# Performance work log

Measured on AMD Instinct MI355X. Metric: run time of the kernel, lower is better.

The kernel has to match this reference:

```python
import jax, jax.numpy as jnp
import numpy as np


def setup_inputs() -> dict:
    key = jax.random.key(0)
    k1, k2 = jax.random.split(key)
    B, N, D, O = 16, 2048, 512, 512
    x = jax.random.normal(k1, (B, N, D), dtype=jnp.float32)
    # original uses nn.init.uniform_ -> U[0,1)
    kernel = jax.random.uniform(k2, (3, D, O), dtype=jnp.float32)
    return {"x": x, "kernel": kernel}


def reference(x, kernel):
    # x: [B, N, D], kernel: [3, D, O]
    O = kernel.shape[-1]
    q = jnp.einsum("bnd,do->bno", x, kernel[0])
    k = jnp.einsum("bnd,do->bno", x, kernel[1])
    v = jnp.einsum("bnd,do->bno", x, kernel[2])
    scores = jnp.einsum("bqo,bko->bqk", q, k) / jnp.sqrt(jnp.float32(O))
    attn = jax.nn.softmax(scores, axis=-1)  # [B, N, N]
    return jnp.einsum("bqk,bko->bqo", attn, v)
```

## Files before the change

### kernel.cpp

```cpp
#include <hip/hip_runtime.h>
#include <hip/hip_bf16.h>

typedef __bf16 bf16_t;
typedef _Float16 f16_t;
typedef __bf16 bf16x8 __attribute__((ext_vector_type(8)));
typedef _Float16 f16x8 __attribute__((ext_vector_type(8)));
typedef float  f32x4  __attribute__((ext_vector_type(4)));

#define GAS __attribute__((address_space(1)))
#define LAS __attribute__((address_space(3)))

__device__ __forceinline__ void gload_lds16(const void* g, void* l) {
    __builtin_amdgcn_global_load_lds((const GAS void*)g, (LAS void*)l, 16, 0, 0);
}

#define QSCALE 0.044194173824159216f
#define L2E    1.4426950408889634f

__global__ __launch_bounds__(256) void k_split_x(const float* __restrict__ X,
                                                 bf16_t* __restrict__ H,
                                                 bf16_t* __restrict__ L, int n) {
    int i = (blockIdx.x * 256 + threadIdx.x) * 4;
    if (i >= n) return;
    float4 v = *(const float4*)(X + i);
    float vv[4] = {v.x, v.y, v.z, v.w};
    union { bf16_t b[4]; uint2 u; } hh, ll;
#pragma unroll
    for (int j = 0; j < 4; j++) {
        bf16_t h = (bf16_t)vv[j];
        hh.b[j] = h;
        ll.b[j] = (bf16_t)(vv[j] - (float)h);
    }
    *(uint2*)(H + i) = hh.u;
    *(uint2*)(L + i) = ll.u;
}

__global__ __launch_bounds__(256) void k_split_wt(const float* __restrict__ W,
                                                  bf16_t* __restrict__ H,
                                                  bf16_t* __restrict__ L) {
    int t = blockIdx.x * 256 + threadIdx.x;
    int base = t * 4;
    int m = base >> 18;
    int o = (base >> 9) & 511;
    int d = base & 511;
    union { bf16_t b[4]; uint2 u; } hh, ll;
#pragma unroll
    for (int j = 0; j < 4; j++) {
        float w = W[m * 262144 + (d + j) * 512 + o];
        bf16_t h = (bf16_t)w;
        hh.b[j] = h;
        ll.b[j] = (bf16_t)(w - (float)h);
    }
    *(uint2*)(H + base) = hh.u;
    *(uint2*)(L + base) = ll.u;
}

__global__ __launch_bounds__(256) void k_qkv(
    const bf16_t* __restrict__ Ah, const bf16_t* __restrict__ Al,
    const bf16_t* __restrict__ Bh, const bf16_t* __restrict__ Bl,
    f16_t* __restrict__ Qf,
    f16_t* __restrict__ Kh, f16_t* __restrict__ Kl,
    bf16_t* __restrict__ VT) {
    __shared__ bf16_t lds[16384];
    bf16_t* As_h = lds;
    bf16_t* Bs_h = lds + 4096;
    bf16_t* As_l = lds + 8192;
    bf16_t* Bs_l = lds + 12288;

    const int tid = threadIdx.x;
    const int lane = tid & 63;
    const int wid = tid >> 6;
    const int wr = wid >> 1, wc = wid & 1;
    const size_t i0 = (size_t)blockIdx.y * 128;
    const size_t j0 = (size_t)blockIdx.x * 128;

    const bf16_t* pAh = Ah + i0 * 512;
    const bf16_t* pBh = Bh + j0 * 512;
    const bf16_t* pAl = Al + i0 * 512;
    const bf16_t* pBl = Bl + j0 * 512;

    const int srow = tid >> 2;
    const int scoff = (tid & 3) * 8;

    f32x4 acc[4][4] = {};

    const int arow = wr * 64 + (lane & 15);
    const int brow = wc * 64 + (lane & 15);
    const int ko = (lane >> 4) * 8;

    for (int kt = 0; kt < 512; kt += 32) {
#pragma unroll
        for (int c = 0; c < 2; c++) {
            const size_t ra = (size_t)(c * 64 + srow) * 512 + kt + scoff;
            const int loff = c * 2048 + tid * 8;
            gload_lds16(pAh + ra, As_h + loff);
            gload_lds16(pBh + ra, Bs_h + loff);
            gload_lds16(pAl + ra, As_l + loff);
            gload_lds16(pBl + ra, Bs_l + loff);
        }
        __syncthreads();

        bf16x8 ah[4], bh[4], al[4], bl[4];
#pragma unroll
        for (int m = 0; m < 4; m++) ah[m] = *(const bf16x8*)&As_h[(arow + m * 16) * 32 + ko];
#pragma unroll
        for (int n = 0; n < 4; n++) bh[n] = *(const bf16x8*)&Bs_h[(brow + n * 16) * 32 + ko];
#pragma unroll
        for (int m = 0; m < 4; m++) al[m] = *(const bf16x8*)&As_l[(arow + m * 16) * 32 + ko];
#pragma unroll
        for (int n = 0; n < 4; n++) bl[n] = *(const bf16x8*)&Bs_l[(brow + n * 16) * 32 + ko];
        __builtin_amdgcn_s_setprio(1);
#pragma unroll
        for (int m = 0; m < 4; m++)
#pragma unroll
            for (int n = 0; n < 4; n++) {
                acc[m][n] = __builtin_amdgcn_mfma_f32_16x16x32_bf16(ah[m], bh[n], acc[m][n], 0, 0, 0);
                acc[m][n] = __builtin_amdgcn_mfma_f32_16x16x32_bf16(ah[m], bl[n], acc[m][n], 0, 0, 0);
                acc[m][n] = __builtin_amdgcn_mfma_f32_16x16x32_bf16(al[m], bh[n], acc[m][n], 0, 0, 0);
            }
        __builtin_amdgcn_s_setprio(0);
        __syncthreads();
    }

#pragma unroll
    for (int m = 0; m < 4; m++) {
#pragma unroll
        for (int n = 0; n < 4; n++) {
#pragma unroll
            for (int j = 0; j < 4; j++) {
                const size_t gr = i0 + wr * 64 + m * 16 + (lane >> 4) * 4 + j;
                const size_t gc = j0 + wc * 64 + n * 16 + (lane & 15);
                float v = acc[m][n][j];
                const int mat = (int)(gc >> 9);
                const size_t bloc = gr >> 11;
                const size_t nrow = gr & 2047;
                const size_t o = gc & 511;
                const size_t idx = bloc * 1048576 + nrow * 512 + o;
                if (mat == 0) {
                    Qf[idx] = (f16_t)(v * QSCALE);
                } else if (mat == 1) {
                    f16_t h = (f16_t)v;
                    Kh[idx] = h; Kl[idx] = (f16_t)(v - (float)h);
                } else {
                    VT[bloc * 1048576 + o * 2048 + nrow] = (bf16_t)v;
                }
            }
        }
    }
}

#define KB_SZ   32768
#define VT_OFF  65536
#define PT_OFF  131072
#define MP_OFF  139264
#define SP_OFF  139776
#define MR_OFF  140288

__global__ __launch_bounds__(512) void k_flash(
    const f16_t* __restrict__ Qf,
    const f16_t* __restrict__ Kh, const f16_t* __restrict__ Kl,
    const bf16_t* __restrict__ VT, float* __restrict__ Out) {
    __shared__ __align__(16) char smem[140800];

    const int tid = threadIdx.x;
    const int l = tid & 63, wid = tid >> 6;
    const int l15 = l & 15, l4 = l >> 4;
    const int rg4 = wid >> 1, kg = wid & 1;
    const int rg2 = wid >> 2, cg = wid & 3;

    const int total = gridDim.x * gridDim.y;
    const int f = blockIdx.x + gridDim.x * blockIdx.y;
    const int fp = (f & 7) * (total >> 3) + (f >> 3);
    const int b = fp >> 5;
    const int q0 = (fp & 31) * 64;
    const size_t NB = 1048576;

    const f16_t* qfb = Qf + (size_t)b * NB;
    const f16_t* khb = Kh + (size_t)b * NB;
    const f16_t* klb = Kl + (size_t)b * NB;
    const bf16_t* vtb = VT + (size_t)b * NB;

    float* MP = (float*)(smem + MP_OFF);
    float* SP = (float*)(smem + SP_OFF);
    float* MR = (float*)(smem + MR_OFF);

    if (tid < 128) MR[tid] = -3e38f;

    f32x4 O[2][8] = {};
    float mreg[2][4], lreg[2][4];
#pragma unroll
    for (int mf = 0; mf < 2; mf++)
#pragma unroll
        for (int j = 0; j < 4; j++) { mreg[mf][j] = -3e38f; lreg[mf][j] = 0.f; }

    const int srow = tid >> 3;
    const int sgl = (tid & 7) ^ (srow & 7);
    const int gsw = l15 & 7;

    auto stage_k = [&](int t, int kc2, int b2) {
#pragma unroll
        for (int sub = 0; sub < 2; sub++) {
            const int co = kc2 * 128 + sub * 64 + sgl * 8;
            f16_t* d = (f16_t*)(smem + b2 * KB_SZ + sub * 16384) + tid * 8;
            gload_lds16(khb + (size_t)(t * 64 + srow) * 512 + co, d);
            gload_lds16(klb + (size_t)(t * 64 + srow) * 512 + co, d + 4096);
        }
    };
    auto stage_v = [&](int t, int j) {
        const int g = j * 512 + tid;
        const int orow = g >> 3;
        const int gl = (g & 7) ^ (orow & 7);
        gload_lds16(vtb + (size_t)orow * 2048 + t * 64 + gl * 8,
                    (bf16_t*)(smem + VT_OFF + g * 16));
    };

#pragma unroll
    for (int qc = 0; qc < 8; qc++) {
        const int co = qc * 64 + sgl * 8;
        gload_lds16(qfb + (size_t)(q0 + srow) * 512 + co,
                    (f16_t*)(smem + VT_OFF + qc * 8192) + tid * 8);
    }
    stage_k(0, 0, 0);
    asm volatile("s_waitcnt vmcnt(4)" ::: "memory");
    __builtin_amdgcn_s_barrier();

    f16x8 qreg[16];
    const int arow = rg4 * 16 + l15;
#pragma unroll
    for (int qc = 0; qc < 8; qc++)
#pragma unroll
        for (int ks = 0; ks < 2; ks++) {
            const int gph = ((ks * 4 + l4) ^ gsw) << 4;
            qreg[qc * 2 + ks] = *(const f16x8*)(smem + VT_OFF + qc * 8192 + arow * 128 + gph);
        }
    asm volatile("s_waitcnt lgkmcnt(0)" ::: "memory");
    __builtin_amdgcn_s_barrier();

#pragma unroll 1
    for (int t = 0; t < 32; t++) {
        f32x4 S[2] = {};
#pragma unroll
        for (int kc2 = 0; kc2 < 4; kc2++) {
            if (kc2 == 0) asm volatile("s_waitcnt vmcnt(0)" ::: "memory");
            else          asm volatile("s_waitcnt vmcnt(2)" ::: "memory");
            __builtin_amdgcn_s_barrier();
            if (kc2 < 3) {
                stage_k(t, kc2 + 1, (kc2 + 1) & 1);
                stage_v(t, kc2 * 2);
                stage_v(t, kc2 * 2 + 1);
            } else {
                stage_v(t, 6);
                stage_v(t, 7);
                if (t < 31) stage_k(t + 1, 0, 0);
            }
            const char* CB = smem + (kc2 & 1) * KB_SZ;
#pragma unroll
            for (int sub = 0; sub < 2; sub++)
#pragma unroll
                for (int ks = 0; ks < 2; ks++) {
                    const int gph = ((ks * 4 + l4) ^ gsw) << 4;
                    f16x8 qa = qreg[kc2 * 4 + sub * 2 + ks];
                    __builtin_amdgcn_s_setprio(1);
#pragma unroll
                    for (int nf = 0; nf < 2; nf++) {
                        const int brow = kg * 32 + nf * 16 + l15;
                        f16x8 bh = *(const f16x8*)(CB + sub * 16384 + brow * 128 + gph);
                        f16x8 bl = *(const f16x8*)(CB + sub * 16384 + 8192 + brow * 128 + gph);
                        S[nf] = __builtin_amdgcn_mfma_f32_16x16x32_f16(qa, bh, S[nf], 0, 0, 0);
                        S[nf] = __builtin_amdgcn_mfma_f32_16x16x32_f16(qa, bl, S[nf], 0, 0, 0);
                    }
                    __builtin_amdgcn_s_setprio(0);
                }
        }

        const int rb4 = rg4 * 16 + l4 * 4;
        float pm[4];
#pragma unroll
        for (int j = 0; j < 4; j++) pm[j] = fmaxf(S[0][j], S[1][j]);
#pragma unroll
        for (int off = 1; off < 16; off <<= 1)
#pragma unroll
            for (int j = 0; j < 4; j++) pm[j] = fmaxf(pm[j], __shfl_xor(pm[j], off));
        if (l15 == 0) {
            f32x4 v; v[0] = pm[0]; v[1] = pm[1]; v[2] = pm[2]; v[3] = pm[3];
            *(f32x4*)(MP + kg * 64 + rb4) = v;
        }
        asm volatile("s_waitcnt lgkmcnt(0)" ::: "memory");
        __builtin_amdgcn_s_barrier();

        f32x4 mp0 = *(const f32x4*)(MP + rb4);
        f32x4 mp1 = *(const f32x4*)(MP + 64 + rb4);
        f32x4 mold = *(const f32x4*)(MR + (t & 1) * 64 + rb4);
        float mnew[4];
#pragma unroll
        for (int j = 0; j < 4; j++) mnew[j] = fmaxf(mold[j], fmaxf(mp0[j], mp1[j]));
        if (kg == 0 && l15 == 0) {
            f32x4 v; v[0] = mnew[0]; v[1] = mnew[1]; v[2] = mnew[2]; v[3] = mnew[3];
            *(f32x4*)(MR + ((t + 1) & 1) * 64 + rb4) = v;
        }
        float p[2][4], ps[4];
#pragma unroll
        for (int nf = 0; nf < 2; nf++)
#pragma unroll
            for (int j = 0; j < 4; j++) p[nf][j] = exp2f((S[nf][j] - mnew[j]) * L2E);
#pragma unroll
        for (int j = 0; j < 4; j++) ps[j] = p[0][j] + p[1][j];
#pragma unroll
        for (int off = 1; off < 16; off <<= 1)
#pragma unroll
            for (int j = 0; j < 4; j++) ps[j] += __shfl_xor(ps[j], off);
        if (l15 == 0) {
            f32x4 v; v[0] = ps[0]; v[1] = ps[1]; v[2] = ps[2]; v[3] = ps[3];
            *(f32x4*)(SP + kg * 64 + rb4) = v;
        }
#pragma unroll
        for (int nf = 0; nf < 2; nf++)
#pragma unroll
            for (int j = 0; j < 4; j++) {
                const int row = rb4 + j;
                const int phys = (kg * 4 + nf * 2 + (l15 >> 3)) ^ (row & 7);
                *(bf16_t*)(smem + PT_OFF + row * 128 + phys * 16 + (l15 & 7) * 2) =
                    (bf16_t)p[nf][j];
            }
        if (t < 31) asm volatile("s_waitcnt vmcnt(4) lgkmcnt(0)" ::: "memory");
        else        asm volatile("s_waitcnt vmcnt(0) lgkmcnt(0)" ::: "memory");
        __builtin_amdgcn_s_barrier();

#pragma unroll
        for (int mf = 0; mf < 2; mf++) {
            const int rb = rg2 * 32 + mf * 16 + l4 * 4;
            f32x4 mn = *(const f32x4*)(MR + ((t + 1) & 1) * 64 + rb);
            f32x4 sp0 = *(const f32x4*)(SP + rb);
            f32x4 sp1 = *(const f32x4*)(SP + 64 + rb);
            float fr[4];
#pragma unroll
            for (int j = 0; j < 4; j++) {
                fr[j] = exp2f((mreg[mf][j] - mn[j]) * L2E);
                lreg[mf][j] = lreg[mf][j] * fr[j] + sp0[j] + sp1[j];
                mreg[mf][j] = mn[j];
            }
#pragma unroll
            for (int nf = 0; nf < 8; nf++)
#pragma unroll
                for (int j = 0; j < 4; j++) O[mf][nf][j] *= fr[j];
        }
#pragma unroll
        for (int ks = 0; ks < 2; ks++) {
            const int gph = ((ks * 4 + l4) ^ gsw) << 4;
            bf16x8 pa[2];
#pragma unroll
            for (int mf = 0; mf < 2; mf++) {
                const int prow = rg2 * 32 + mf * 16 + l15;
                pa[mf] = *(const bf16x8*)(smem + PT_OFF + prow * 128 + gph);
            }
            __builtin_amdgcn_s_setprio(1);
#pragma unroll
            for (int nf = 0; nf < 8; nf++) {
                const int vrow = cg * 128 + nf * 16 + l15;
                bf16x8 vb = *(const bf16x8*)(smem + VT_OFF + vrow * 128 + gph);
#pragma unroll
                for (int mf = 0; mf < 2; mf++)
                    O[mf][nf] = __builtin_amdgcn_mfma_f32_16x16x32_bf16(pa[mf], vb, O[mf][nf], 0, 0, 0);
            }
            __builtin_amdgcn_s_setprio(0);
        }
    }

#pragma unroll
    for (int mf = 0; mf < 2; mf++) {
        float inv[4];
#pragma unroll
        for (int j = 0; j < 4; j++) inv[j] = 1.0f / lreg[mf][j];
#pragma unroll
        for (int nf = 0; nf < 8; nf++)
#pragma unroll
            for (int j = 0; j < 4; j++) {
                const size_t row = q0 + rg2 * 32 + mf * 16 + l4 * 4 + j;
                const size_t col = cg * 128 + nf * 16 + l15;
                Out[(size_t)b * NB + row * 512 + col] = O[mf][nf][j] * inv[j];
            }
    }
}

extern "C" void kernel_launch(void* const* d_in, const int* in_sizes, int n_in,
                              void* d_out, int out_size, void* d_ws, size_t ws_size,
                              hipStream_t stream) {
    const float* x = (const float*)d_in[0];
    const float* w = (const float*)d_in[1];
    float* out = (float*)d_out;

    const size_t NB = (size_t)2048 * 512;
    const size_t NW = (size_t)3 * 512 * 512;

    const size_t perG = 6 * NB * 2;
    size_t fixed = 2 * NW * 2 + 4096;
    int G = 1;
    if (ws_size > fixed + perG) {
        size_t g = (ws_size - fixed) / perG;
        G = (int)(g > 16 ? 16 : g);
    } else {
        return;
    }

    size_t off = 0;
    char* wsb = (char*)d_ws;
    auto take = [&](size_t bytes) -> char* {
        char* p = wsb + off;
        off = (off + bytes + 255) & ~(size_t)255;
        return p;
    };
    bf16_t* wth = (bf16_t*)take(NW * 2);
    bf16_t* wtl = (bf16_t*)take(NW * 2);
    bf16_t* xh = (bf16_t*)take(G * NB * 2);
    bf16_t* xl = (bf16_t*)take(G * NB * 2);
    f16_t*  qf = (f16_t*)take(G * NB * 2);
    f16_t*  kh = (f16_t*)take(G * NB * 2);
    f16_t*  kl = (f16_t*)take(G * NB * 2);
    bf16_t* vt = (bf16_t*)take(G * NB * 2);

    k_split_wt<<<dim3((unsigned)(NW / 4 / 256)), 256, 0, stream>>>(w, wth, wtl);

    for (int g0 = 0; g0 < 16; g0 += G) {
        const int Gc = (16 - g0 < G) ? (16 - g0) : G;
        const size_t base = (size_t)g0 * NB;
        k_split_x<<<dim3((unsigned)(Gc * NB / 4 / 256)), 256, 0, stream>>>(
            x + base, xh, xl, (int)(Gc * NB));
        k_qkv<<<dim3(12, 16 * Gc), 256, 0, stream>>>(
            xh, xl, wth, wtl, qf, kh, kl, vt);
        k_flash<<<dim3(32, Gc), 512, 0, stream>>>(
            qf, kh, kl, vt, out + base);
    }
}
```

Before: 568.1 us.

## Store K low residual as scaled FP8 and skip split-precision MFMAs for V

The low-order residual of K is stored as FP8 scaled by 256 instead of FP16. The score correction term is computed with an fp8×fp8 MFMA using an FP8 copy of Q, which halves the bytes of the Kl stream and the LDS footprint. Separately, the QKV GEMM blocks that produce V now skip loading the low-precision halves and the two correction MFMAs, since V is stored only as bf16. The aim is to cut memory traffic and MFMA work, at the cost of lower precision in the QK^T correction term and more complex LDS addressing.

```diff
diff --git a/kernel.cpp b/kernel.cpp
--- a/kernel.cpp
+++ b/kernel.cpp
@@ -59,7 +59,7 @@
     const bf16_t* __restrict__ Ah, const bf16_t* __restrict__ Al,
     const bf16_t* __restrict__ Bh, const bf16_t* __restrict__ Bl,
     f16_t* __restrict__ Qf,
-    f16_t* __restrict__ Kh, f16_t* __restrict__ Kl,
+    f16_t* __restrict__ Kh, unsigned char* __restrict__ Kl8,
     bf16_t* __restrict__ VT) {
     __shared__ bf16_t lds[16384];
     bf16_t* As_h = lds;
@@ -73,6 +73,8 @@
     const int wr = wid >> 1, wc = wid & 1;
     const size_t i0 = (size_t)blockIdx.y * 128;
     const size_t j0 = (size_t)blockIdx.x * 128;
+    const int mat3 = (int)(j0 >> 9);
+    const bool full = (mat3 != 2);
 
     const bf16_t* pAh = Ah + i0 * 512;
     const bf16_t* pBh = Bh + j0 * 512;
@@ -95,30 +97,43 @@
             const int loff = c * 2048 + tid * 8;
             gload_lds16(pAh + ra, As_h + loff);
             gload_lds16(pBh + ra, Bs_h + loff);
-            gload_lds16(pAl + ra, As_l + loff);
-            gload_lds16(pBl + ra, Bs_l + loff);
+            if (full) {
+                gload_lds16(pAl + ra, As_l + loff);
+                gload_lds16(pBl + ra, Bs_l + loff);
+            }
         }
         __syncthreads();
 
-        bf16x8 ah[4], bh[4], al[4], bl[4];
+        bf16x8 ah[4], bh[4];
 #pragma unroll
         for (int m = 0; m < 4; m++) ah[m] = *(const bf16x8*)&As_h[(arow + m * 16) * 32 + ko];
 #pragma unroll
         for (int n = 0; n < 4; n++) bh[n] = *(const bf16x8*)&Bs_h[(brow + n * 16) * 32 + ko];
-#pragma unroll
-        for (int m = 0; m < 4; m++) al[m] = *(const bf16x8*)&As_l[(arow + m * 16) * 32 + ko];
-#pragma unroll
-        for (int n = 0; n < 4; n++) bl[n] = *(const bf16x8*)&Bs_l[(brow + n * 16) * 32 + ko];
-        __builtin_amdgcn_s_setprio(1);
-#pragma unroll
-        for (int m = 0; m < 4; m++)
-#pragma unroll
-            for (int n = 0; n < 4; n++) {
-                acc[m][n] = __builtin_amdgcn_mfma_f32_16x16x32_bf16(ah[m], bh[n], acc[m][n], 0, 0, 0);
-                acc[m][n] = __builtin_amdgcn_mfma_f32_16x16x32_bf16(ah[m], bl[n], acc[m][n], 0, 0, 0);
-                acc[m][n] = __builtin_amdgcn_mfma_f32_16x16x32_bf16(al[m], bh[n], acc[m][n], 0, 0, 0);
-            }
-        __builtin_amdgcn_s_setprio(0);
+        if (full) {
+            bf16x8 al[4], bl[4];
+#pragma unroll
+            for (int m = 0; m < 4; m++) al[m] = *(const bf16x8*)&As_l[(arow + m * 16) * 32 + ko];
+#pragma unroll
+            for (int n = 0; n < 4; n++) bl[n] = *(const bf16x8*)&Bs_l[(brow + n * 16) * 32 + ko];
+            __builtin_amdgcn_s_setprio(1);
+#pragma unroll
+            for (int m = 0; m < 4; m++)
+#pragma unroll
+                for (int n = 0; n < 4; n++) {
+                    acc[m][n] = __builtin_amdgcn_mfma_f32_16x16x32_bf16(ah[m], bh[n], acc[m][n], 0, 0, 0);
+                    acc[m][n] = __builtin_amdgcn_mfma_f32_16x16x32_bf16(ah[m], bl[n], acc[m][n], 0, 0, 0);
+                    acc[m][n] = __builtin_amdgcn_mfma_f32_16x16x32_bf16(al[m], bh[n], acc[m][n], 0, 0, 0);
+                }
+            __builtin_amdgcn_s_setprio(0);
+        } else {
+            __builtin_amdgcn_s_setprio(1);
+#pragma unroll
+            for (int m = 0; m < 4; m++)
+#pragma unroll
+                for (int n = 0; n < 4; n++)
+                    acc[m][n] = __builtin_amdgcn_mfma_f32_16x16x32_bf16(ah[m], bh[n], acc[m][n], 0, 0, 0);
+            __builtin_amdgcn_s_setprio(0);
+        }
         __syncthreads();
     }
 
@@ -131,16 +146,18 @@
                 const size_t gr = i0 + wr * 64 + m * 16 + (lane >> 4) * 4 + j;
                 const size_t gc = j0 + wc * 64 + n * 16 + (lane & 15);
                 float v = acc[m][n][j];
-                const int mat = (int)(gc >> 9);
                 const size_t bloc = gr >> 11;
                 const size_t nrow = gr & 2047;
                 const size_t o = gc & 511;
                 const size_t idx = bloc * 1048576 + nrow * 512 + o;
-                if (mat == 0) {
+                if (mat3 == 0) {
                     Qf[idx] = (f16_t)(v * QSCALE);
-                } else if (mat == 1) {
+                } else if (mat3 == 1) {
                     f16_t h = (f16_t)v;
-                    Kh[idx] = h; Kl[idx] = (f16_t)(v - (float)h);
+                    Kh[idx] = h;
+                    float lo = (v - (float)h) * 256.0f;
+                    int p = __builtin_amdgcn_cvt_pk_fp8_f32(lo, lo, 0, false);
+                    Kl8[idx] = (unsigned char)(p & 0xff);
                 } else {
                     VT[bloc * 1048576 + o * 2048 + nrow] = (bf16_t)v;
                 }
@@ -149,18 +166,18 @@
     }
 }
 
-#define KB_SZ   32768
-#define VT_OFF  65536
-#define PT_OFF  131072
-#define MP_OFF  139264
-#define SP_OFF  139776
-#define MR_OFF  140288
+#define KB_SZ   24576
+#define VT_OFF  49152
+#define PT_OFF  114688
+#define MP_OFF  122880
+#define SP_OFF  123392
+#define MR_OFF  123904
 
 __global__ __launch_bounds__(512) void k_flash(
     const f16_t* __restrict__ Qf,
-    const f16_t* __restrict__ Kh, const f16_t* __restrict__ Kl,
+    const f16_t* __restrict__ Kh, const unsigned char* __restrict__ Kl8,
     const bf16_t* __restrict__ VT, float* __restrict__ Out) {
-    __shared__ __align__(16) char smem[140800];
+    __shared__ __align__(16) char smem[124416];
 
     const int tid = threadIdx.x;
     const int l = tid & 63, wid = tid >> 6;
@@ -177,7 +194,7 @@
 
     const f16_t* qfb = Qf + (size_t)b * NB;
     const f16_t* khb = Kh + (size_t)b * NB;
-    const f16_t* klb = Kl + (size_t)b * NB;
+    const unsigned char* kl8b = Kl8 + (size_t)b * NB;
     const bf16_t* vtb = VT + (size_t)b * NB;
 
     float* MP = (float*)(smem + MP_OFF);
@@ -201,10 +218,11 @@
 #pragma unroll
         for (int sub = 0; sub < 2; sub++) {
             const int co = kc2 * 128 + sub * 64 + sgl * 8;
-            f16_t* d = (f16_t*)(smem + b2 * KB_SZ + sub * 16384) + tid * 8;
-            gload_lds16(khb + (size_t)(t * 64 + srow) * 512 + co, d);
-            gload_lds16(klb + (size_t)(t * 64 + srow) * 512 + co, d + 4096);
-        }
+            gload_lds16(khb + (size_t)(t * 64 + srow) * 512 + co,
+                        (f16_t*)(smem + b2 * KB_SZ + sub * 8192) + tid * 8);
+        }
+        gload_lds16(kl8b + (size_t)(t * 64 + srow) * 512 + kc2 * 128 + sgl * 16,
+                    (char*)(smem + b2 * KB_SZ + 16384) + tid * 16);
     };
     auto stage_v = [&](int t, int j) {
         const int g = j * 512 + tid;
@@ -221,7 +239,7 @@
                     (f16_t*)(smem + VT_OFF + qc * 8192) + tid * 8);
     }
     stage_k(0, 0, 0);
-    asm volatile("s_waitcnt vmcnt(4)" ::: "memory");
+    asm volatile("s_waitcnt vmcnt(3)" ::: "memory");
     __builtin_amdgcn_s_barrier();
 
     f16x8 qreg[16];
@@ -233,12 +251,23 @@
             const int gph = ((ks * 4 + l4) ^ gsw) << 4;
             qreg[qc * 2 + ks] = *(const f16x8*)(smem + VT_OFF + qc * 8192 + arow * 128 + gph);
         }
+    long q8reg[16];
+#pragma unroll
+    for (int i = 0; i < 16; i++) {
+        int w0 = 0, w1 = 0;
+        w0 = __builtin_amdgcn_cvt_pk_fp8_f32((float)qreg[i][0], (float)qreg[i][1], w0, false);
+        w0 = __builtin_amdgcn_cvt_pk_fp8_f32((float)qreg[i][2], (float)qreg[i][3], w0, true);
+        w1 = __builtin_amdgcn_cvt_pk_fp8_f32((float)qreg[i][4], (float)qreg[i][5], w1, false);
+        w1 = __builtin_amdgcn_cvt_pk_fp8_f32((float)qreg[i][6], (float)qreg[i][7], w1, true);
+        int2 pk; pk.x = w0; pk.y = w1;
+        q8reg[i] = __builtin_bit_cast(long, pk);
+    }
     asm volatile("s_waitcnt lgkmcnt(0)" ::: "memory");
     __builtin_amdgcn_s_barrier();
 
 #pragma unroll 1
     for (int t = 0; t < 32; t++) {
-        f32x4 S[2] = {};
+        f32x4 S[2] = {}, S2[2] = {};
 #pragma unroll
         for (int kc2 = 0; kc2 < 4; kc2++) {
             if (kc2 == 0) asm volatile("s_waitcnt vmcnt(0)" ::: "memory");
@@ -260,18 +289,25 @@
                 for (int ks = 0; ks < 2; ks++) {
                     const int gph = ((ks * 4 + l4) ^ gsw) << 4;
                     f16x8 qa = qreg[kc2 * 4 + sub * 2 + ks];
+                    long a8 = q8reg[kc2 * 4 + sub * 2 + ks];
                     __builtin_amdgcn_s_setprio(1);
 #pragma unroll
                     for (int nf = 0; nf < 2; nf++) {
                         const int brow = kg * 32 + nf * 16 + l15;
-                        f16x8 bh = *(const f16x8*)(CB + sub * 16384 + brow * 128 + gph);
-                        f16x8 bl = *(const f16x8*)(CB + sub * 16384 + 8192 + brow * 128 + gph);
+                        f16x8 bh = *(const f16x8*)(CB + sub * 8192 + brow * 128 + gph);
+                        long b8 = *(const long*)(CB + 16384 + brow * 128 +
+                                   ((((sub << 2) + (ks << 1) + (l4 >> 1)) ^ gsw) << 4) +
+                                   ((l4 & 1) << 3));
                         S[nf] = __builtin_amdgcn_mfma_f32_16x16x32_f16(qa, bh, S[nf], 0, 0, 0);
-                        S[nf] = __builtin_amdgcn_mfma_f32_16x16x32_f16(qa, bl, S[nf], 0, 0, 0);
+                        S2[nf] = __builtin_amdgcn_mfma_f32_16x16x32_fp8_fp8(a8, b8, S2[nf], 0, 0, 0);
                     }
                     __builtin_amdgcn_s_setprio(0);
                 }
         }
+#pragma unroll
+        for (int nf = 0; nf < 2; nf++)
+#pragma unroll
+            for (int j = 0; j < 4; j++) S[nf][j] += S2[nf][j] * 0.00390625f;
 
         const int rb4 = rg4 * 16 + l4 * 4;
         float pm[4];
@@ -322,7 +358,7 @@
                 *(bf16_t*)(smem + PT_OFF + row * 128 + phys * 16 + (l15 & 7) * 2) =
                     (bf16_t)p[nf][j];
             }
-        if (t < 31) asm volatile("s_waitcnt vmcnt(4) lgkmcnt(0)" ::: "memory");
+        if (t < 31) asm volatile("s_waitcnt vmcnt(3) lgkmcnt(0)" ::: "memory");
         else        asm volatile("s_waitcnt vmcnt(0) lgkmcnt(0)" ::: "memory");
         __builtin_amdgcn_s_barrier();
 
@@ -392,7 +428,7 @@
     const size_t NB = (size_t)2048 * 512;
     const size_t NW = (size_t)3 * 512 * 512;
 
-    const size_t perG = 6 * NB * 2;
+    const size_t perG = 11 * NB;
     size_t fixed = 2 * NW * 2 + 4096;
     int G = 1;
     if (ws_size > fixed + perG) {
@@ -415,7 +451,7 @@
     bf16_t* xl = (bf16_t*)take(G * NB * 2);
     f16_t*  qf = (f16_t*)take(G * NB * 2);
     f16_t*  kh = (f16_t*)take(G * NB * 2);
-    f16_t*  kl = (f16_t*)take(G * NB * 2);
+    unsigned char* kl8 = (unsigned char*)take(G * NB);
     bf16_t* vt = (bf16_t*)take(G * NB * 2);
 
     k_split_wt<<<dim3((unsigned)(NW / 4 / 256)), 256, 0, stream>>>(w, wth, wtl);
@@ -426,8 +462,8 @@
         k_split_x<<<dim3((unsigned)(Gc * NB / 4 / 256)), 256, 0, stream>>>(
             x + base, xh, xl, (int)(Gc * NB));
         k_qkv<<<dim3(12, 16 * Gc), 256, 0, stream>>>(
-            xh, xl, wth, wtl, qf, kh, kl, vt);
+            xh, xl, wth, wtl, qf, kh, kl8, vt);
         k_flash<<<dim3(32, Gc), 512, 0, stream>>>(
-            qf, kh, kl, vt, out + base);
-    }
-}
+            qf, kh, kl8, vt, out + base);
+    }
+}
```

After: 670.3 us. 18.0% more time.
